# Performance work log

Hardware: AMD Instinct MI355X
Metric: run time of the kernel (lower is better)

Reference implementation:

```python
import jax, jax.numpy as jnp
import numpy as np

M, K, N = 4096, 4096, 11008

def setup_inputs() -> dict:
    key = jax.random.key(0)
    k1, k2, k3, k4 = jax.random.split(key, 4)
    x = jax.random.normal(k1, (M, K), dtype=jnp.float32)
    weight = jax.random.randint(k2, (K, N), 0, 127, dtype=jnp.int32)
    antiquant_scale = jax.random.uniform(k3, (N,), dtype=jnp.float32)
    antiquant_offset = jax.random.normal(k4, (N,), dtype=jnp.float32)
    return {"x": x, "weight": weight, "antiquant_scale": antiquant_scale, "antiquant_offset": antiquant_offset}

def reference(x, weight, antiquant_scale, antiquant_offset):
    # Dequantize: (w + offset) * scale, per output channel (broadcast over K)
    dequantized_weight = (weight.astype(jnp.float32) + antiquant_offset) * antiquant_scale  # [K, N]
    return jnp.matmul(x, dequantized_weight)  # [M, N]
```

## Files before the change

kernel.cpp:

```cpp
#include <hip/hip_runtime.h>
#include <hip/hip_bf16.h>
#include <stdint.h>

#define M_DIM 4096
#define K_DIM 4096
#define N_DIM 11008
#define BKT 64
#define NT (K_DIM / BKT)
#define GRID_MN 688
#define NBLK_M 16

typedef __attribute__((ext_vector_type(8))) short short8;
typedef __attribute__((ext_vector_type(4))) float floatx4;

__device__ __forceinline__ short f2bf(float f) {
  union { float f; uint32_t u; } c; c.f = f;
  uint32_t u = c.u;
  u += 0x7FFFu + ((u >> 16) & 1u);
  return (short)(u >> 16);
}

__device__ __forceinline__ void gload_lds16(const void* g, void* l) {
  __builtin_amdgcn_global_load_lds(
      (const __attribute__((address_space(1))) unsigned int*)g,
      (__attribute__((address_space(3))) unsigned int*)l, 16, 0, 0);
}

__global__ __launch_bounds__(256) void convert_x_kernel(const float* __restrict__ x,
                                                        short* __restrict__ xb,
                                                        float* __restrict__ rowsum) {
  const int m = blockIdx.x;
  const int t = threadIdx.x;
  const float* row = x + (size_t)m * K_DIM + t * 16;
  short* orow = xb + (size_t)m * K_DIM + t * 16;
  float4 v0 = *(const float4*)(row + 0);
  float4 v1 = *(const float4*)(row + 4);
  float4 v2 = *(const float4*)(row + 8);
  float4 v3 = *(const float4*)(row + 12);
  float sum = v0.x + v0.y + v0.z + v0.w
            + v1.x + v1.y + v1.z + v1.w
            + v2.x + v2.y + v2.z + v2.w
            + v3.x + v3.y + v3.z + v3.w;
  short8 o0, o1;
  o0[0] = f2bf(v0.x); o0[1] = f2bf(v0.y); o0[2] = f2bf(v0.z); o0[3] = f2bf(v0.w);
  o0[4] = f2bf(v1.x); o0[5] = f2bf(v1.y); o0[6] = f2bf(v1.z); o0[7] = f2bf(v1.w);
  o1[0] = f2bf(v2.x); o1[1] = f2bf(v2.y); o1[2] = f2bf(v2.z); o1[3] = f2bf(v2.w);
  o1[4] = f2bf(v3.x); o1[5] = f2bf(v3.y); o1[6] = f2bf(v3.z); o1[7] = f2bf(v3.w);
  *(short8*)(orow) = o0;
  *(short8*)(orow + 8) = o1;
  #pragma unroll
  for (int off = 32; off > 0; off >>= 1) sum += __shfl_down(sum, off);
  __shared__ float part[4];
  if ((t & 63) == 0) part[t >> 6] = sum;
  __syncthreads();
  if (t == 0) rowsum[m] = part[0] + part[1] + part[2] + part[3];
}

__global__ __launch_bounds__(256) void convert_w_kernel(const int* __restrict__ w,
                                                        short* __restrict__ wt) {
  __shared__ short tile[64][72];
  const int bk = blockIdx.x * 64;
  const int bn = blockIdx.y * 64;
  const int t = threadIdx.x;
  const int kr = t >> 2;
  const int c0 = (t & 3) * 16;
  const int* src = w + (size_t)(bk + kr) * N_DIM + bn + c0;
  int4 a = *(const int4*)(src + 0);
  int4 b = *(const int4*)(src + 4);
  int4 c = *(const int4*)(src + 8);
  int4 d = *(const int4*)(src + 12);
  short* dst = &tile[kr][c0];
  dst[0]  = f2bf((float)a.x); dst[1]  = f2bf((float)a.y);
  dst[2]  = f2bf((float)a.z); dst[3]  = f2bf((float)a.w);
  dst[4]  = f2bf((float)b.x); dst[5]  = f2bf((float)b.y);
  dst[6]  = f2bf((float)b.z); dst[7]  = f2bf((float)b.w);
  dst[8]  = f2bf((float)c.x); dst[9]  = f2bf((float)c.y);
  dst[10] = f2bf((float)c.z); dst[11] = f2bf((float)c.w);
  dst[12] = f2bf((float)d.x); dst[13] = f2bf((float)d.y);
  dst[14] = f2bf((float)d.z); dst[15] = f2bf((float)d.w);
  __syncthreads();
  const int nr = t >> 2;
  short8 o0, o1;
  #pragma unroll
  for (int j = 0; j < 8; ++j) o0[j] = tile[c0 + j][nr];
  #pragma unroll
  for (int j = 0; j < 8; ++j) o1[j] = tile[c0 + 8 + j][nr];
  short* odst = wt + (size_t)(bn + nr) * K_DIM + bk + c0;
  *(short8*)(odst) = o0;
  *(short8*)(odst + 8) = o1;
}

__global__ __launch_bounds__(512, 2) void gemm_kernel(const short* __restrict__ xb,
                                                      const short* __restrict__ wt,
                                                      const float* __restrict__ scale,
                                                      const float* __restrict__ offset,
                                                      const float* __restrict__ rowsum,
                                                      float* __restrict__ out) {
  __shared__ short lds[2][4][8192];
  const int tid = threadIdx.x;
  const int bid = blockIdx.x;
  const int wg = (bid & 7) * (GRID_MN / 8) + (bid >> 3);
  const int bm = (wg % NBLK_M) * 256;
  const int bn = (wg / NBLK_M) * 256;

  const int wid = tid >> 6;
  const int lane = tid & 63;
  const int wr = wid >> 2;
  const int wc = wid & 3;
  const int hb = wc >> 1;
  const int lr = lane & 15;
  const int lg = lane >> 4;
  const int swz = lr & 7;
  const int gk0 = (lg ^ swz) * 8;
  const int gk1 = ((lg ^ 4) ^ swz) * 8;
  const int brow = (wc & 1) * 64 + lr;

  const int srow = tid >> 3;
  const int glog = (tid & 7) ^ (srow & 7);

  auto stage = [&](const short* opbase, int rowbase, int half, int kt, short* region) {
    const short* s0 = opbase + (size_t)(rowbase + half * 128 + srow) * K_DIM + kt * BKT + glog * 8;
    gload_lds16(s0, (char*)region + tid * 16);
    const short* s1 = opbase + (size_t)(rowbase + half * 128 + srow + 64) * K_DIM + kt * BKT + glog * 8;
    gload_lds16(s1, (char*)region + (tid + 512) * 16);
  };

  floatx4 acc[8][4];
  const floatx4 zero = {0.f, 0.f, 0.f, 0.f};
  #pragma unroll
  for (int i = 0; i < 8; ++i)
    #pragma unroll
    for (int j = 0; j < 4; ++j) acc[i][j] = zero;

  stage(xb, bm, 0, 0, &lds[0][0][0]);
  stage(xb, bm, 1, 0, &lds[0][1][0]);
  stage(wt, bn, 0, 0, &lds[0][2][0]);
  stage(wt, bn, 1, 0, &lds[0][3][0]);
  asm volatile("s_waitcnt vmcnt(4)" ::: "memory");
  stage(wt, bn, 0, 1, &lds[1][2][0]);
  stage(wt, bn, 1, 1, &lds[1][3][0]);
  stage(xb, bm, 0, 1, &lds[1][0][0]);
  asm volatile("s_waitcnt vmcnt(6)" ::: "memory");
  __builtin_amdgcn_s_barrier();

  for (int c = 0; c < NT; ++c) {
    const int beta = c & 1;
    const short* As = &lds[beta][wr][0];
    const short* Bs = &lds[beta][2 + hb][0];
    short8 af[4][2], b0[2][2], b1[2][2];

    #pragma unroll
    for (int mf = 0; mf < 4; ++mf) {
      const short* p = As + (mf * 16 + lr) * 64;
      af[mf][0] = *(const short8*)(p + gk0);
      af[mf][1] = *(const short8*)(p + gk1);
    }
    #pragma unroll
    for (int nf = 0; nf < 2; ++nf) {
      const short* p = Bs + (brow + nf * 16) * 64;
      b0[nf][0] = *(const short8*)(p + gk0);
      b0[nf][1] = *(const short8*)(p + gk1);
      const short* q = Bs + (brow + (nf + 2) * 16) * 64;
      b1[nf][0] = *(const short8*)(q + gk0);
      b1[nf][1] = *(const short8*)(q + gk1);
    }
    if (c + 1 < NT) stage(xb, bm, 1, c + 1, &lds[beta ^ 1][1][0]);
    asm volatile("s_waitcnt lgkmcnt(8)" ::: "memory");
    __builtin_amdgcn_s_barrier();
    asm volatile("s_waitcnt lgkmcnt(0)" ::: "memory");
    __builtin_amdgcn_s_setprio(1);
    #pragma unroll
    for (int mf = 0; mf < 4; ++mf)
      #pragma unroll
      for (int nf = 0; nf < 2; ++nf) {
        acc[mf][nf] = __builtin_amdgcn_mfma_f32_16x16x32_bf16(af[mf][0], b0[nf][0], acc[mf][nf], 0, 0, 0);
        acc[mf][nf] = __builtin_amdgcn_mfma_f32_16x16x32_bf16(af[mf][1], b0[nf][1], acc[mf][nf], 0, 0, 0);
      }
    __builtin_amdgcn_s_setprio(0);
    __builtin_amdgcn_s_barrier();

    if (c + 2 < NT) stage(wt, bn, 0, c + 2, &lds[beta][2][0]);
    __builtin_amdgcn_s_barrier();
    asm volatile("s_waitcnt lgkmcnt(0)" ::: "memory");
    __builtin_amdgcn_s_setprio(1);
    #pragma unroll
    for (int mf = 0; mf < 4; ++mf)
      #pragma unroll
      for (int nf = 0; nf < 2; ++nf) {
        acc[mf][nf + 2] = __builtin_amdgcn_mfma_f32_16x16x32_bf16(af[mf][0], b1[nf][0], acc[mf][nf + 2], 0, 0, 0);
        acc[mf][nf + 2] = __builtin_amdgcn_mfma_f32_16x16x32_bf16(af[mf][1], b1[nf][1], acc[mf][nf + 2], 0, 0, 0);
      }
    __builtin_amdgcn_s_setprio(0);
    __builtin_amdgcn_s_barrier();

    #pragma unroll
    for (int mf = 0; mf < 4; ++mf) {
      const short* p = As + ((mf + 4) * 16 + lr) * 64;
      af[mf][0] = *(const short8*)(p + gk0);
      af[mf][1] = *(const short8*)(p + gk1);
    }
    if (c + 2 < NT) stage(wt, bn, 1, c + 2, &lds[beta][3][0]);
    __builtin_amdgcn_s_barrier();
    asm volatile("s_waitcnt lgkmcnt(0)" ::: "memory");
    __builtin_amdgcn_s_setprio(1);
    #pragma unroll
    for (int mf = 0; mf < 4; ++mf)
      #pragma unroll
      for (int nf = 0; nf < 2; ++nf) {
        acc[mf + 4][nf] = __builtin_amdgcn_mfma_f32_16x16x32_bf16(af[mf][0], b0[nf][0], acc[mf + 4][nf], 0, 0, 0);
        acc[mf + 4][nf] = __builtin_amdgcn_mfma_f32_16x16x32_bf16(af[mf][1], b0[nf][1], acc[mf + 4][nf], 0, 0, 0);
      }
    __builtin_amdgcn_s_setprio(0);
    __builtin_amdgcn_s_barrier();

    if (c + 2 < NT) {
      stage(xb, bm, 0, c + 2, &lds[beta][0][0]);
      asm volatile("s_waitcnt vmcnt(6)" ::: "memory");
    } else {
      asm volatile("s_waitcnt vmcnt(0)" ::: "memory");
    }
    __builtin_amdgcn_s_barrier();
    asm volatile("s_waitcnt lgkmcnt(0)" ::: "memory");
    __builtin_amdgcn_s_setprio(1);
    #pragma unroll
    for (int mf = 0; mf < 4; ++mf)
      #pragma unroll
      for (int nf = 0; nf < 2; ++nf) {
        acc[mf + 4][nf + 2] = __builtin_amdgcn_mfma_f32_16x16x32_bf16(af[mf][0], b1[nf][0], acc[mf + 4][nf + 2], 0, 0, 0);
        acc[mf + 4][nf + 2] = __builtin_amdgcn_mfma_f32_16x16x32_bf16(af[mf][1], b1[nf][1], acc[mf + 4][nf + 2], 0, 0, 0);
      }
    __builtin_amdgcn_s_setprio(0);
    __builtin_amdgcn_s_barrier();
  }

  const int orow0 = bm + wr * 128 + lg * 4;
  const int ocol0 = bn + wc * 64 + lr;
  float rs[8][4];
  #pragma unroll
  for (int amf = 0; amf < 8; ++amf)
    #pragma unroll
    for (int r = 0; r < 4; ++r)
      rs[amf][r] = rowsum[orow0 + amf * 16 + r];
  #pragma unroll
  for (int anf = 0; anf < 4; ++anf) {
    const int n = ocol0 + anf * 16;
    const float s = scale[n];
    const float o = offset[n];
    #pragma unroll
    for (int amf = 0; amf < 8; ++amf) {
      const int mbase = orow0 + amf * 16;
      #pragma unroll
      for (int r = 0; r < 4; ++r) {
        out[(size_t)(mbase + r) * N_DIM + n] = (acc[amf][anf][r] + o * rs[amf][r]) * s;
      }
    }
  }
}

__global__ __launch_bounds__(256) void fallback_gemm(const float* __restrict__ x,
                                                     const int* __restrict__ w,
                                                     const float* __restrict__ scale,
                                                     const float* __restrict__ offset,
                                                     float* __restrict__ out) {
  __shared__ float xs[32][33];
  __shared__ float bs[32][33];
  const int bm = blockIdx.y * 32, bn = blockIdx.x * 32;
  const int t = threadIdx.x;
  const int tm = t >> 5, tn = t & 31;
  float acc[4] = {0.f, 0.f, 0.f, 0.f};
  for (int k0 = 0; k0 < K_DIM; k0 += 32) {
    #pragma unroll
    for (int i = 0; i < 4; ++i) {
      int idx = t + i * 256; int r = idx >> 5, c = idx & 31;
      xs[r][c] = x[(size_t)(bm + r) * K_DIM + k0 + c];
      bs[r][c] = ((float)w[(size_t)(k0 + r) * N_DIM + bn + c] + offset[bn + c]) * scale[bn + c];
    }
    __syncthreads();
    #pragma unroll 8
    for (int kk = 0; kk < 32; ++kk) {
      float wv = bs[kk][tn];
      #pragma unroll
      for (int i = 0; i < 4; ++i) acc[i] += xs[tm + 8 * i][kk] * wv;
    }
    __syncthreads();
  }
  #pragma unroll
  for (int i = 0; i < 4; ++i)
    out[(size_t)(bm + tm + 8 * i) * N_DIM + bn + tn] = acc[i];
}

extern "C" void kernel_launch(void* const* d_in, const int* in_sizes, int n_in,
                              void* d_out, int out_size, void* d_ws, size_t ws_size,
                              hipStream_t stream) {
  const float* x      = (const float*)d_in[0];
  const int*   w      = (const int*)d_in[1];
  const float* scale  = (const float*)d_in[2];
  const float* offset = (const float*)d_in[3];
  float* out = (float*)d_out;

  const size_t xb_bytes = (size_t)M_DIM * K_DIM * 2;
  const size_t wt_bytes = (size_t)N_DIM * K_DIM * 2;
  const size_t rs_bytes = (size_t)M_DIM * 4;

  if (ws_size >= xb_bytes + wt_bytes + rs_bytes) {
    short* xb = (short*)d_ws;
    short* wt = (short*)((char*)d_ws + xb_bytes);
    float* rowsum = (float*)((char*)d_ws + xb_bytes + wt_bytes);
    convert_x_kernel<<<M_DIM, 256, 0, stream>>>(x, xb, rowsum);
    convert_w_kernel<<<dim3(K_DIM / 64, N_DIM / 64), 256, 0, stream>>>(w, wt);
    gemm_kernel<<<GRID_MN, 512, 0, stream>>>(xb, wt, scale, offset, rowsum, out);
  } else {
    fallback_gemm<<<dim3(N_DIM / 32, M_DIM / 32), 256, 0, stream>>>(x, w, scale, offset, out);
  }
}
```

Measured before the change: 415.7 us.

## Make GEMM persistent with cross-tile prefetch and reordered MFMA phases

Launches a fixed grid of 256 persistent workgroups, each looping over 2 or 3 output tiles. The software pipeline is carried across tile boundaries so the next tile's first K-slices load while the current tile finishes. The four MFMA phases are reordered so A halves and B halves are loaded at different points, and the epilogue reads rowsum as float4. This aims to remove the partial last wave from 688 blocks on 256 CUs and the per-block pipeline ramp. In exchange the 688 tiles split unevenly (2 vs 3 per workgroup), and the epilogue now sits inside the main loop.

```diff
diff --git a/kernel.cpp b/kernel.cpp
--- a/kernel.cpp
+++ b/kernel.cpp
@@ -9,6 +9,7 @@
 #define NT (K_DIM / BKT)
 #define GRID_MN 688
 #define NBLK_M 16
+#define NWG 256
 
 typedef __attribute__((ext_vector_type(8))) short short8;
 typedef __attribute__((ext_vector_type(4))) float floatx4;
@@ -98,10 +99,16 @@
                                                       float* __restrict__ out) {
   __shared__ short lds[2][4][8192];
   const int tid = threadIdx.x;
-  const int bid = blockIdx.x;
-  const int wg = (bid & 7) * (GRID_MN / 8) + (bid >> 3);
-  const int bm = (wg % NBLK_M) * 256;
-  const int bn = (wg / NBLK_M) * 256;
+  const int w = blockIdx.x;
+  const int swz0 = (w & 7) * 32 + (w >> 3);
+  const int cnt = (swz0 < (GRID_MN - 2 * NWG)) ? 3 : 2;
+  const int S = cnt * NT;
+
+  int bmCur = (swz0 & 15) * 256;
+  int bnCur = (swz0 >> 4) * 256;
+  int TNext = swz0 + NWG;
+  int bmNext = (TNext & 15) * 256;
+  int bnNext = (TNext >> 4) * 256;
 
   const int wid = tid >> 6;
   const int lane = tid & 63;
@@ -118,10 +125,10 @@
   const int srow = tid >> 3;
   const int glog = (tid & 7) ^ (srow & 7);
 
-  auto stage = [&](const short* opbase, int rowbase, int half, int kt, short* region) {
-    const short* s0 = opbase + (size_t)(rowbase + half * 128 + srow) * K_DIM + kt * BKT + glog * 8;
+  auto stage = [&](const short* opbase, int rowbase, int half, int ktile, short* region) {
+    const short* s0 = opbase + (size_t)(rowbase + half * 128 + srow) * K_DIM + ktile * BKT + glog * 8;
     gload_lds16(s0, (char*)region + tid * 16);
-    const short* s1 = opbase + (size_t)(rowbase + half * 128 + srow + 64) * K_DIM + kt * BKT + glog * 8;
+    const short* s1 = opbase + (size_t)(rowbase + half * 128 + srow + 64) * K_DIM + ktile * BKT + glog * 8;
     gload_lds16(s1, (char*)region + (tid + 512) * 16);
   };
 
@@ -132,40 +139,88 @@
     #pragma unroll
     for (int j = 0; j < 4; ++j) acc[i][j] = zero;
 
-  stage(xb, bm, 0, 0, &lds[0][0][0]);
-  stage(xb, bm, 1, 0, &lds[0][1][0]);
-  stage(wt, bn, 0, 0, &lds[0][2][0]);
-  stage(wt, bn, 1, 0, &lds[0][3][0]);
-  asm volatile("s_waitcnt vmcnt(4)" ::: "memory");
-  stage(wt, bn, 0, 1, &lds[1][2][0]);
-  stage(wt, bn, 1, 1, &lds[1][3][0]);
-  stage(xb, bm, 0, 1, &lds[1][0][0]);
+  stage(xb, bmCur, 0, 0, &lds[0][0][0]);
+  stage(xb, bmCur, 1, 0, &lds[0][1][0]);
+  stage(wt, bnCur, 0, 0, &lds[0][2][0]);
+  stage(wt, bnCur, 1, 0, &lds[0][3][0]);
+  stage(xb, bmCur, 0, 1, &lds[1][0][0]);
+  stage(wt, bnCur, 0, 1, &lds[1][2][0]);
+  stage(wt, bnCur, 1, 1, &lds[1][3][0]);
   asm volatile("s_waitcnt vmcnt(6)" ::: "memory");
   __builtin_amdgcn_s_barrier();
 
-  for (int c = 0; c < NT; ++c) {
-    const int beta = c & 1;
+  for (int s = 0; s < S; ++s) {
+    const int beta = s & 1;
+    const int kt = s & 63;
     const short* As = &lds[beta][wr][0];
     const short* Bs = &lds[beta][2 + hb][0];
-    short8 af[4][2], b0[2][2], b1[2][2];
+    short8 a03[4][2], a47[4][2], b0[2][2], b1[2][2];
 
     #pragma unroll
     for (int mf = 0; mf < 4; ++mf) {
       const short* p = As + (mf * 16 + lr) * 64;
-      af[mf][0] = *(const short8*)(p + gk0);
-      af[mf][1] = *(const short8*)(p + gk1);
+      a03[mf][0] = *(const short8*)(p + gk0);
+      a03[mf][1] = *(const short8*)(p + gk1);
     }
     #pragma unroll
     for (int nf = 0; nf < 2; ++nf) {
       const short* p = Bs + (brow + nf * 16) * 64;
       b0[nf][0] = *(const short8*)(p + gk0);
       b0[nf][1] = *(const short8*)(p + gk1);
+    }
+    asm volatile("s_waitcnt lgkmcnt(8)" ::: "memory");
+    __builtin_amdgcn_s_barrier();
+    asm volatile("s_waitcnt lgkmcnt(0)" ::: "memory");
+    __builtin_amdgcn_s_setprio(1);
+    #pragma unroll
+    for (int mf = 0; mf < 4; ++mf)
+      #pragma unroll
+      for (int nf = 0; nf < 2; ++nf) {
+        acc[mf][nf] = __builtin_amdgcn_mfma_f32_16x16x32_bf16(a03[mf][0], b0[nf][0], acc[mf][nf], 0, 0, 0);
+        acc[mf][nf] = __builtin_amdgcn_mfma_f32_16x16x32_bf16(a03[mf][1], b0[nf][1], acc[mf][nf], 0, 0, 0);
+      }
+    __builtin_amdgcn_s_setprio(0);
+    __builtin_amdgcn_s_barrier();
+
+    #pragma unroll
+    for (int mf = 0; mf < 4; ++mf) {
+      const short* p = As + ((mf + 4) * 16 + lr) * 64;
+      a47[mf][0] = *(const short8*)(p + gk0);
+      a47[mf][1] = *(const short8*)(p + gk1);
+    }
+    {
+      const int t1 = s + 1;
+      if (t1 < S) {
+        const int rb = ((t1 >> 6) != (s >> 6)) ? bmNext : bmCur;
+        stage(xb, rb, 1, t1 & 63, &lds[beta ^ 1][1][0]);
+      }
+    }
+    __builtin_amdgcn_s_barrier();
+    asm volatile("s_waitcnt lgkmcnt(0)" ::: "memory");
+    __builtin_amdgcn_s_setprio(1);
+    #pragma unroll
+    for (int mf = 0; mf < 4; ++mf)
+      #pragma unroll
+      for (int nf = 0; nf < 2; ++nf) {
+        acc[mf + 4][nf] = __builtin_amdgcn_mfma_f32_16x16x32_bf16(a47[mf][0], b0[nf][0], acc[mf + 4][nf], 0, 0, 0);
+        acc[mf + 4][nf] = __builtin_amdgcn_mfma_f32_16x16x32_bf16(a47[mf][1], b0[nf][1], acc[mf + 4][nf], 0, 0, 0);
+      }
+    __builtin_amdgcn_s_setprio(0);
+    __builtin_amdgcn_s_barrier();
+
+    #pragma unroll
+    for (int nf = 0; nf < 2; ++nf) {
       const short* q = Bs + (brow + (nf + 2) * 16) * 64;
       b1[nf][0] = *(const short8*)(q + gk0);
       b1[nf][1] = *(const short8*)(q + gk1);
     }
-    if (c + 1 < NT) stage(xb, bm, 1, c + 1, &lds[beta ^ 1][1][0]);
-    asm volatile("s_waitcnt lgkmcnt(8)" ::: "memory");
+    {
+      const int t2 = s + 2;
+      if (t2 < S) {
+        const int rb = ((t2 >> 6) != (s >> 6)) ? bmNext : bmCur;
+        stage(xb, rb, 0, t2 & 63, &lds[beta][0][0]);
+      }
+    }
     __builtin_amdgcn_s_barrier();
     asm volatile("s_waitcnt lgkmcnt(0)" ::: "memory");
     __builtin_amdgcn_s_setprio(1);
@@ -173,13 +228,23 @@
     for (int mf = 0; mf < 4; ++mf)
       #pragma unroll
       for (int nf = 0; nf < 2; ++nf) {
-        acc[mf][nf] = __builtin_amdgcn_mfma_f32_16x16x32_bf16(af[mf][0], b0[nf][0], acc[mf][nf], 0, 0, 0);
-        acc[mf][nf] = __builtin_amdgcn_mfma_f32_16x16x32_bf16(af[mf][1], b0[nf][1], acc[mf][nf], 0, 0, 0);
+        acc[mf][nf + 2] = __builtin_amdgcn_mfma_f32_16x16x32_bf16(a03[mf][0], b1[nf][0], acc[mf][nf + 2], 0, 0, 0);
+        acc[mf][nf + 2] = __builtin_amdgcn_mfma_f32_16x16x32_bf16(a03[mf][1], b1[nf][1], acc[mf][nf + 2], 0, 0, 0);
       }
     __builtin_amdgcn_s_setprio(0);
     __builtin_amdgcn_s_barrier();
 
-    if (c + 2 < NT) stage(wt, bn, 0, c + 2, &lds[beta][2][0]);
+    {
+      const int t2 = s + 2;
+      if (t2 < S) {
+        const int rb = ((t2 >> 6) != (s >> 6)) ? bnNext : bnCur;
+        stage(wt, rb, 0, t2 & 63, &lds[beta][2][0]);
+        stage(wt, rb, 1, t2 & 63, &lds[beta][3][0]);
+        asm volatile("s_waitcnt vmcnt(6)" ::: "memory");
+      } else {
+        asm volatile("s_waitcnt vmcnt(0)" ::: "memory");
+      }
+    }
     __builtin_amdgcn_s_barrier();
     asm volatile("s_waitcnt lgkmcnt(0)" ::: "memory");
     __builtin_amdgcn_s_setprio(1);
@@ -187,72 +252,42 @@
     for (int mf = 0; mf < 4; ++mf)
       #pragma unroll
       for (int nf = 0; nf < 2; ++nf) {
-        acc[mf][nf + 2] = __builtin_amdgcn_mfma_f32_16x16x32_bf16(af[mf][0], b1[nf][0], acc[mf][nf + 2], 0, 0, 0);
-        acc[mf][nf + 2] = __builtin_amdgcn_mfma_f32_16x16x32_bf16(af[mf][1], b1[nf][1], acc[mf][nf + 2], 0, 0, 0);
+        acc[mf + 4][nf + 2] = __builtin_amdgcn_mfma_f32_16x16x32_bf16(a47[mf][0], b1[nf][0], acc[mf + 4][nf + 2], 0, 0, 0);
+        acc[mf + 4][nf + 2] = __builtin_amdgcn_mfma_f32_16x16x32_bf16(a47[mf][1], b1[nf][1], acc[mf + 4][nf + 2], 0, 0, 0);
       }
     __builtin_amdgcn_s_setprio(0);
     __builtin_amdgcn_s_barrier();
 
-    #pragma unroll
-    for (int mf = 0; mf < 4; ++mf) {
-      const short* p = As + ((mf + 4) * 16 + lr) * 64;
-      af[mf][0] = *(const short8*)(p + gk0);
-      af[mf][1] = *(const short8*)(p + gk1);
-    }
-    if (c + 2 < NT) stage(wt, bn, 1, c + 2, &lds[beta][3][0]);
-    __builtin_amdgcn_s_barrier();
-    asm volatile("s_waitcnt lgkmcnt(0)" ::: "memory");
-    __builtin_amdgcn_s_setprio(1);
-    #pragma unroll
-    for (int mf = 0; mf < 4; ++mf)
-      #pragma unroll
-      for (int nf = 0; nf < 2; ++nf) {
-        acc[mf + 4][nf] = __builtin_amdgcn_mfma_f32_16x16x32_bf16(af[mf][0], b0[nf][0], acc[mf + 4][nf], 0, 0, 0);
-        acc[mf + 4][nf] = __builtin_amdgcn_mfma_f32_16x16x32_bf16(af[mf][1], b0[nf][1], acc[mf + 4][nf], 0, 0, 0);
-      }
-    __builtin_amdgcn_s_setprio(0);
-    __builtin_amdgcn_s_barrier();
-
-    if (c + 2 < NT) {
-      stage(xb, bm, 0, c + 2, &lds[beta][0][0]);
-      asm volatile("s_waitcnt vmcnt(6)" ::: "memory");
-    } else {
-      asm volatile("s_waitcnt vmcnt(0)" ::: "memory");
-    }
-    __builtin_amdgcn_s_barrier();
-    asm volatile("s_waitcnt lgkmcnt(0)" ::: "memory");
-    __builtin_amdgcn_s_setprio(1);
-    #pragma unroll
-    for (int mf = 0; mf < 4; ++mf)
-      #pragma unroll
-      for (int nf = 0; nf < 2; ++nf) {
-        acc[mf + 4][nf + 2] = __builtin_amdgcn_mfma_f32_16x16x32_bf16(af[mf][0], b1[nf][0], acc[mf + 4][nf + 2], 0, 0, 0);
-        acc[mf + 4][nf + 2] = __builtin_amdgcn_mfma_f32_16x16x32_bf16(af[mf][1], b1[nf][1], acc[mf + 4][nf + 2], 0, 0, 0);
-      }
-    __builtin_amdgcn_s_setprio(0);
-    __builtin_amdgcn_s_barrier();
-  }
-
-  const int orow0 = bm + wr * 128 + lg * 4;
-  const int ocol0 = bn + wc * 64 + lr;
-  float rs[8][4];
-  #pragma unroll
-  for (int amf = 0; amf < 8; ++amf)
-    #pragma unroll
-    for (int r = 0; r < 4; ++r)
-      rs[amf][r] = rowsum[orow0 + amf * 16 + r];
-  #pragma unroll
-  for (int anf = 0; anf < 4; ++anf) {
-    const int n = ocol0 + anf * 16;
-    const float s = scale[n];
-    const float o = offset[n];
-    #pragma unroll
-    for (int amf = 0; amf < 8; ++amf) {
-      const int mbase = orow0 + amf * 16;
-      #pragma unroll
-      for (int r = 0; r < 4; ++r) {
-        out[(size_t)(mbase + r) * N_DIM + n] = (acc[amf][anf][r] + o * rs[amf][r]) * s;
-      }
+    if (kt == 63) {
+      const int orow0 = bmCur + wr * 128 + lg * 4;
+      const int ocol0 = bnCur + wc * 64 + lr;
+      float4 rsv[8];
+      #pragma unroll
+      for (int amf = 0; amf < 8; ++amf)
+        rsv[amf] = *(const float4*)&rowsum[orow0 + amf * 16];
+      #pragma unroll
+      for (int anf = 0; anf < 4; ++anf) {
+        const int n = ocol0 + anf * 16;
+        const float sc = scale[n];
+        const float of = offset[n];
+        #pragma unroll
+        for (int amf = 0; amf < 8; ++amf) {
+          const int mbase = orow0 + amf * 16;
+          const float4 rv = rsv[amf];
+          out[(size_t)(mbase + 0) * N_DIM + n] = (acc[amf][anf][0] + of * rv.x) * sc;
+          out[(size_t)(mbase + 1) * N_DIM + n] = (acc[amf][anf][1] + of * rv.y) * sc;
+          out[(size_t)(mbase + 2) * N_DIM + n] = (acc[amf][anf][2] + of * rv.z) * sc;
+          out[(size_t)(mbase + 3) * N_DIM + n] = (acc[amf][anf][3] + of * rv.w) * sc;
+        }
+      }
+      #pragma unroll
+      for (int i = 0; i < 8; ++i)
+        #pragma unroll
+        for (int j = 0; j < 4; ++j) acc[i][j] = zero;
+      bmCur = bmNext; bnCur = bnNext;
+      TNext += NWG;
+      bmNext = (TNext & 15) * 256;
+      bnNext = (TNext >> 4) * 256;
     }
   }
 }
@@ -308,7 +343,7 @@
     float* rowsum = (float*)((char*)d_ws + xb_bytes + wt_bytes);
     convert_x_kernel<<<M_DIM, 256, 0, stream>>>(x, xb, rowsum);
     convert_w_kernel<<<dim3(K_DIM / 64, N_DIM / 64), 256, 0, stream>>>(w, wt);
-    gemm_kernel<<<GRID_MN, 512, 0, stream>>>(xb, wt, scale, offset, rowsum, out);
+    gemm_kernel<<<NWG, 512, 0, stream>>>(xb, wt, scale, offset, rowsum, out);
   } else {
     fallback_gemm<<<dim3(N_DIM / 32, M_DIM / 32), 256, 0, stream>>>(x, w, scale, offset, out);
   }
```

After: 452.1 us. 8.8% more time.

## Software-pipeline A fragment LDS reads across iterations and reorder MFMA quadrants

Applied to the files above, without the earlier changes.

Keeps both halves of the A fragments in separate register sets and prefetches the first half for the next K-step during the last MFMA phase of the current one. The quadrant order changes to (a03,b0), (a47,b0), (a03,b1), (a47,b1), and the global-to-LDS stage order and waitcnt placement are reshuffled to match. The aim is to hide LDS read latency behind MFMAs and remove one lgkmcnt wait per phase. It costs extra VGPRs for the doubled A fragments, and the changed barrier and waitcnt ordering risks hazards or lower occupancy. The epilogue also reads the rowsum values as float4 instead of scalars.

```diff
diff --git a/kernel.cpp b/kernel.cpp
--- a/kernel.cpp
+++ b/kernel.cpp
@@ -136,25 +136,28 @@
   stage(xb, bm, 1, 0, &lds[0][1][0]);
   stage(wt, bn, 0, 0, &lds[0][2][0]);
   stage(wt, bn, 1, 0, &lds[0][3][0]);
-  asm volatile("s_waitcnt vmcnt(4)" ::: "memory");
   stage(wt, bn, 0, 1, &lds[1][2][0]);
+  stage(xb, bm, 0, 1, &lds[1][0][0]);
   stage(wt, bn, 1, 1, &lds[1][3][0]);
-  stage(xb, bm, 0, 1, &lds[1][0][0]);
   asm volatile("s_waitcnt vmcnt(6)" ::: "memory");
   __builtin_amdgcn_s_barrier();
 
-  for (int c = 0; c < NT; ++c) {
-    const int beta = c & 1;
+  short8 a03[4][2], a47[4][2], b0[2][2], b1[2][2];
+  {
+    const short* As = &lds[0][wr][0];
+    #pragma unroll
+    for (int mf = 0; mf < 4; ++mf) {
+      const short* p = As + (mf * 16 + lr) * 64;
+      a03[mf][0] = *(const short8*)(p + gk0);
+      a03[mf][1] = *(const short8*)(p + gk1);
+    }
+  }
+
+  for (int s = 0; s < NT; ++s) {
+    const int beta = s & 1;
     const short* As = &lds[beta][wr][0];
     const short* Bs = &lds[beta][2 + hb][0];
-    short8 af[4][2], b0[2][2], b1[2][2];
-
-    #pragma unroll
-    for (int mf = 0; mf < 4; ++mf) {
-      const short* p = As + (mf * 16 + lr) * 64;
-      af[mf][0] = *(const short8*)(p + gk0);
-      af[mf][1] = *(const short8*)(p + gk1);
-    }
+
     #pragma unroll
     for (int nf = 0; nf < 2; ++nf) {
       const short* p = Bs + (brow + nf * 16) * 64;
@@ -164,8 +167,8 @@
       b1[nf][0] = *(const short8*)(q + gk0);
       b1[nf][1] = *(const short8*)(q + gk1);
     }
-    if (c + 1 < NT) stage(xb, bm, 1, c + 1, &lds[beta ^ 1][1][0]);
     asm volatile("s_waitcnt lgkmcnt(8)" ::: "memory");
+    if (s + 1 < NT) stage(xb, bm, 1, s + 1, &lds[beta ^ 1][1][0]);
     __builtin_amdgcn_s_barrier();
     asm volatile("s_waitcnt lgkmcnt(0)" ::: "memory");
     __builtin_amdgcn_s_setprio(1);
@@ -173,13 +176,19 @@
     for (int mf = 0; mf < 4; ++mf)
       #pragma unroll
       for (int nf = 0; nf < 2; ++nf) {
-        acc[mf][nf] = __builtin_amdgcn_mfma_f32_16x16x32_bf16(af[mf][0], b0[nf][0], acc[mf][nf], 0, 0, 0);
-        acc[mf][nf] = __builtin_amdgcn_mfma_f32_16x16x32_bf16(af[mf][1], b0[nf][1], acc[mf][nf], 0, 0, 0);
+        acc[mf][nf] = __builtin_amdgcn_mfma_f32_16x16x32_bf16(a03[mf][0], b0[nf][0], acc[mf][nf], 0, 0, 0);
+        acc[mf][nf] = __builtin_amdgcn_mfma_f32_16x16x32_bf16(a03[mf][1], b0[nf][1], acc[mf][nf], 0, 0, 0);
       }
     __builtin_amdgcn_s_setprio(0);
     __builtin_amdgcn_s_barrier();
 
-    if (c + 2 < NT) stage(wt, bn, 0, c + 2, &lds[beta][2][0]);
+    #pragma unroll
+    for (int mf = 0; mf < 4; ++mf) {
+      const short* p = As + ((mf + 4) * 16 + lr) * 64;
+      a47[mf][0] = *(const short8*)(p + gk0);
+      a47[mf][1] = *(const short8*)(p + gk1);
+    }
+    if (s + 2 < NT) stage(wt, bn, 0, s + 2, &lds[beta][2][0]);
     __builtin_amdgcn_s_barrier();
     asm volatile("s_waitcnt lgkmcnt(0)" ::: "memory");
     __builtin_amdgcn_s_setprio(1);
@@ -187,47 +196,48 @@
     for (int mf = 0; mf < 4; ++mf)
       #pragma unroll
       for (int nf = 0; nf < 2; ++nf) {
-        acc[mf][nf + 2] = __builtin_amdgcn_mfma_f32_16x16x32_bf16(af[mf][0], b1[nf][0], acc[mf][nf + 2], 0, 0, 0);
-        acc[mf][nf + 2] = __builtin_amdgcn_mfma_f32_16x16x32_bf16(af[mf][1], b1[nf][1], acc[mf][nf + 2], 0, 0, 0);
+        acc[mf + 4][nf] = __builtin_amdgcn_mfma_f32_16x16x32_bf16(a47[mf][0], b0[nf][0], acc[mf + 4][nf], 0, 0, 0);
+        acc[mf + 4][nf] = __builtin_amdgcn_mfma_f32_16x16x32_bf16(a47[mf][1], b0[nf][1], acc[mf + 4][nf], 0, 0, 0);
       }
     __builtin_amdgcn_s_setprio(0);
     __builtin_amdgcn_s_barrier();
 
-    #pragma unroll
-    for (int mf = 0; mf < 4; ++mf) {
-      const short* p = As + ((mf + 4) * 16 + lr) * 64;
-      af[mf][0] = *(const short8*)(p + gk0);
-      af[mf][1] = *(const short8*)(p + gk1);
-    }
-    if (c + 2 < NT) stage(wt, bn, 1, c + 2, &lds[beta][3][0]);
-    __builtin_amdgcn_s_barrier();
-    asm volatile("s_waitcnt lgkmcnt(0)" ::: "memory");
+    if (s + 2 < NT) stage(xb, bm, 0, s + 2, &lds[beta][0][0]);
+    __builtin_amdgcn_s_barrier();
     __builtin_amdgcn_s_setprio(1);
     #pragma unroll
     for (int mf = 0; mf < 4; ++mf)
       #pragma unroll
       for (int nf = 0; nf < 2; ++nf) {
-        acc[mf + 4][nf] = __builtin_amdgcn_mfma_f32_16x16x32_bf16(af[mf][0], b0[nf][0], acc[mf + 4][nf], 0, 0, 0);
-        acc[mf + 4][nf] = __builtin_amdgcn_mfma_f32_16x16x32_bf16(af[mf][1], b0[nf][1], acc[mf + 4][nf], 0, 0, 0);
+        acc[mf][nf + 2] = __builtin_amdgcn_mfma_f32_16x16x32_bf16(a03[mf][0], b1[nf][0], acc[mf][nf + 2], 0, 0, 0);
+        acc[mf][nf + 2] = __builtin_amdgcn_mfma_f32_16x16x32_bf16(a03[mf][1], b1[nf][1], acc[mf][nf + 2], 0, 0, 0);
       }
     __builtin_amdgcn_s_setprio(0);
     __builtin_amdgcn_s_barrier();
 
-    if (c + 2 < NT) {
-      stage(xb, bm, 0, c + 2, &lds[beta][0][0]);
+    if (s + 2 < NT) {
+      stage(wt, bn, 1, s + 2, &lds[beta][3][0]);
       asm volatile("s_waitcnt vmcnt(6)" ::: "memory");
     } else {
       asm volatile("s_waitcnt vmcnt(0)" ::: "memory");
     }
     __builtin_amdgcn_s_barrier();
-    asm volatile("s_waitcnt lgkmcnt(0)" ::: "memory");
+    if (s + 1 < NT) {
+      const short* An = &lds[beta ^ 1][wr][0];
+      #pragma unroll
+      for (int mf = 0; mf < 4; ++mf) {
+        const short* p = An + (mf * 16 + lr) * 64;
+        a03[mf][0] = *(const short8*)(p + gk0);
+        a03[mf][1] = *(const short8*)(p + gk1);
+      }
+    }
     __builtin_amdgcn_s_setprio(1);
     #pragma unroll
     for (int mf = 0; mf < 4; ++mf)
       #pragma unroll
       for (int nf = 0; nf < 2; ++nf) {
-        acc[mf + 4][nf + 2] = __builtin_amdgcn_mfma_f32_16x16x32_bf16(af[mf][0], b1[nf][0], acc[mf + 4][nf + 2], 0, 0, 0);
-        acc[mf + 4][nf + 2] = __builtin_amdgcn_mfma_f32_16x16x32_bf16(af[mf][1], b1[nf][1], acc[mf + 4][nf + 2], 0, 0, 0);
+        acc[mf + 4][nf + 2] = __builtin_amdgcn_mfma_f32_16x16x32_bf16(a47[mf][0], b1[nf][0], acc[mf + 4][nf + 2], 0, 0, 0);
+        acc[mf + 4][nf + 2] = __builtin_amdgcn_mfma_f32_16x16x32_bf16(a47[mf][1], b1[nf][1], acc[mf + 4][nf + 2], 0, 0, 0);
       }
     __builtin_amdgcn_s_setprio(0);
     __builtin_amdgcn_s_barrier();
@@ -235,24 +245,23 @@
 
   const int orow0 = bm + wr * 128 + lg * 4;
   const int ocol0 = bn + wc * 64 + lr;
-  float rs[8][4];
+  float4 rsv[8];
   #pragma unroll
   for (int amf = 0; amf < 8; ++amf)
-    #pragma unroll
-    for (int r = 0; r < 4; ++r)
-      rs[amf][r] = rowsum[orow0 + amf * 16 + r];
+    rsv[amf] = *(const float4*)&rowsum[orow0 + amf * 16];
   #pragma unroll
   for (int anf = 0; anf < 4; ++anf) {
     const int n = ocol0 + anf * 16;
-    const float s = scale[n];
-    const float o = offset[n];
+    const float sc = scale[n];
+    const float of = offset[n];
     #pragma unroll
     for (int amf = 0; amf < 8; ++amf) {
       const int mbase = orow0 + amf * 16;
-      #pragma unroll
-      for (int r = 0; r < 4; ++r) {
-        out[(size_t)(mbase + r) * N_DIM + n] = (acc[amf][anf][r] + o * rs[amf][r]) * s;
-      }
+      const float4 rv = rsv[amf];
+      out[(size_t)(mbase + 0) * N_DIM + n] = (acc[amf][anf][0] + of * rv.x) * sc;
+      out[(size_t)(mbase + 1) * N_DIM + n] = (acc[amf][anf][1] + of * rv.y) * sc;
+      out[(size_t)(mbase + 2) * N_DIM + n] = (acc[amf][anf][2] + of * rv.z) * sc;
+      out[(size_t)(mbase + 3) * N_DIM + n] = (acc[amf][anf][3] + of * rv.w) * sc;
     }
   }
 }
```

Result: no change. 423.6 us (+1.9%).
